# Kernel optimization log

Measured on AMD Instinct MI355X. Metric: run time of the kernel, lower is better.

The kernel has to match this reference:

```python
import jax, jax.numpy as jnp
import numpy as np

D = 256      # embedding_dim
K = 1024     # num_embeddings
B, S = 32, 2048

def setup_inputs() -> dict:
    key = jax.random.key(0)
    k1, k2 = jax.random.split(key)
    inp = jax.random.normal(k1, (B, S, D), dtype=jnp.float32)
    w = jax.random.normal(k2, (D, K), dtype=jnp.float32)  # codebook, [D, K]
    return {"input": inp, "w": w, "weights_loss": 0}


def reference(input, w, weights_loss):
    # flatten tokens: [N, D]
    flat = input.reshape(-1, D)
    N = flat.shape[0]
    # squared euclidean distances to each code: [N, K]
    distances = (jnp.sum(flat * flat, axis=1, keepdims=True)
                 - 2.0 * (flat @ w)
                 + jnp.sum(w * w, axis=0, keepdims=True))
    # nearest code per token (argmax of -dist == argmin of dist)
    flat_idx = jnp.argmax(-distances, axis=1)              # [N] int
    idx = flat_idx.reshape(input.shape[:-1])               # [B, S]
    # embedding gather: w.T is [K, D]
    quantize = jnp.take(w.T, idx, axis=0)                  # [B, S, D]
    # commitment loss: mse(stop_grad(quantize), flat_input)
    q_flat = quantize.reshape(-1, D)
    loss = jnp.mean((jax.lax.stop_gradient(q_flat) - flat) ** 2)
    # straight-through estimator
    quantize_st = input + jax.lax.stop_gradient(quantize - input)
    # one-hot statistics without materializing [N, K]
    dema_cluster_size = jax.ops.segment_sum(
        jnp.ones((N,), dtype=flat.dtype), flat_idx, num_segments=K)  # [K]
    dw = jax.ops.segment_sum(flat, flat_idx, num_segments=K).T       # [D, K]
    avg_probs = dema_cluster_size / N
    perplexity = jnp.exp(-jnp.sum(avg_probs * jnp.log(avg_probs + 1e-10)))
    return (loss,
            quantize_st,
            dema_cluster_size.reshape(1, K),
            dw.reshape(1, D, K),
            idx,
            perplexity)
```

## Files before the change

kernel.cpp:

```cpp
#include <hip/hip_runtime.h>


#define D 256
#define K 1024
#define NTOK 65536

#define OFF_Q   ((size_t)1)
#define OFF_CS  ((size_t)1 + (size_t)NTOK * D)
#define OFF_DW  (OFF_CS + K)
#define OFF_IDX (OFF_DW + (size_t)D * K)
#define OFF_P   (OFF_IDX + NTOK)

#define FLAG_TH  0.05f
#define FLAG_CAP 8192

typedef __attribute__((ext_vector_type(8))) short short8;
typedef __attribute__((ext_vector_type(16))) float f32x16;

__device__ __forceinline__ unsigned short f2bf(float f) {
  unsigned u = __float_as_uint(f);
  return (unsigned short)((u + 0x7FFFu + ((u >> 16) & 1u)) >> 16);
}
__device__ __forceinline__ float bf2f(unsigned short h) {
  return __uint_as_float(((unsigned)h) << 16);
}

__global__ __launch_bounds__(256) void prep_w(const float* __restrict__ w,
                                              float* __restrict__ wT,
                                              unsigned short* __restrict__ whG,
                                              unsigned short* __restrict__ wlG) {
  __shared__ float tile[32][33];
  const int k0 = blockIdx.x * 32, d0 = blockIdx.y * 32;
  const int tx = threadIdx.x, ty = threadIdx.y;
#pragma unroll
  for (int j = 0; j < 4; ++j) {
    const int r = ty + j * 8;
    tile[r][tx] = w[(size_t)(d0 + r) * K + k0 + tx];
  }
  __syncthreads();
#pragma unroll
  for (int j = 0; j < 4; ++j) {
    const int r = ty + j * 8;
    const int k = k0 + r, d = d0 + tx;
    const float v = tile[tx][r];
    wT[(size_t)k * D + d] = v;
    const unsigned short h = f2bf(v);
    const unsigned short l = f2bf(v - bf2f(h));
    const size_t idx = (size_t)(k >> 5) * 8192 +
                       (size_t)(((d >> 4) * 2 + ((d >> 3) & 1)) * 32 + (k & 31)) * 8 +
                       (d & 7);
    whG[idx] = h;
    wlG[idx] = l;
  }
}

__global__ __launch_bounds__(256) void wsq_kernel(const float* __restrict__ wT,
                                                  float* __restrict__ wsq) {
  const int wave = threadIdx.x >> 6, lane = threadIdx.x & 63;
  const int k = blockIdx.x * 4 + wave;
  const float4 v = *(const float4*)(wT + (size_t)k * D + lane * 4);
  float s = v.x * v.x + v.y * v.y + v.z * v.z + v.w * v.w;
#pragma unroll
  for (int m = 1; m < 64; m <<= 1) s += __shfl_xor(s, m);
  if (lane == 0) wsq[k] = s;
}

__global__ __launch_bounds__(256, 2) void vq_score(
    const float* __restrict__ x,
    const unsigned short* __restrict__ whG, const unsigned short* __restrict__ wlG,
    const float* __restrict__ wsq, float* __restrict__ out,
    int* __restrict__ idxInt, int* __restrict__ flagCnt, int* __restrict__ flagged) {
  __shared__ short whS[2][8192];
  __shared__ short wlS[2][8192];
  __shared__ float swsq[K];

  const int tid = threadIdx.x;
#pragma unroll
  for (int j = 0; j < 4; ++j) swsq[tid + j * 256] = wsq[tid + j * 256];

  const int wv = tid >> 6, lane = tid & 63;
  const int col = lane & 31, hi = lane >> 5;
  const int rowG = blockIdx.x * 128 + wv * 32 + col;

  short8 ah[16], al[16];
  {
    const float* xr = x + (size_t)rowG * D + hi * 8;
#pragma unroll
    for (int s = 0; s < 16; ++s) {
      const float4 f0 = *(const float4*)(xr + s * 16);
      const float4 f1 = *(const float4*)(xr + s * 16 + 4);
      const float fv[8] = {f0.x, f0.y, f0.z, f0.w, f1.x, f1.y, f1.z, f1.w};
      short8 a, b;
#pragma unroll
      for (int e = 0; e < 8; ++e) {
        const unsigned short h = f2bf(fv[e]);
        a[e] = (short)h;
        b[e] = (short)f2bf(fv[e] - bf2f(h));
      }
      ah[s] = a;
      al[s] = b;
    }
  }

  auto stage = [&](int chunk, int buf) {
    const short8* srcH = (const short8*)(whG + (size_t)chunk * 8192);
    const short8* srcL = (const short8*)(wlG + (size_t)chunk * 8192);
    short8* dstH = (short8*)whS[buf];
    short8* dstL = (short8*)wlS[buf];
#pragma unroll
    for (int j = 0; j < 4; ++j) {
      dstH[tid + j * 256] = srcH[tid + j * 256];
      dstL[tid + j * 256] = srcL[tid + j * 256];
    }
  };

  float s1[16], s2[16];
  int i1[16];
#pragma unroll
  for (int r = 0; r < 16; ++r) { s1[r] = -3.4e38f; s2[r] = -3.4e38f; i1[r] = 0; }

  stage(0, 0);
  __syncthreads();

  for (int chunk = 0; chunk < 32; ++chunk) {
    const int cur = chunk & 1;
    if (chunk + 1 < 32) stage(chunk + 1, cur ^ 1);

    const short* bhB = whS[cur];
    const short* blB = wlS[cur];
    f32x16 ahh, ahl, alh;
#pragma unroll
    for (int r = 0; r < 16; ++r) { ahh[r] = 0.f; ahl[r] = 0.f; alh[r] = 0.f; }
#pragma unroll
    for (int s = 0; s < 16; ++s) {
      const int off = ((s * 2 + hi) << 8) + (col << 3);
      const short8 bh = *(const short8*)(bhB + off);
      const short8 bl = *(const short8*)(blB + off);
      ahh = __builtin_amdgcn_mfma_f32_32x32x16_bf16(ah[s], bh, ahh, 0, 0, 0);
      ahl = __builtin_amdgcn_mfma_f32_32x32x16_bf16(ah[s], bl, ahl, 0, 0, 0);
      alh = __builtin_amdgcn_mfma_f32_32x32x16_bf16(al[s], bh, alh, 0, 0, 0);
    }

    const int cc = chunk * 32 + col;
    const float wq = swsq[cc];
#pragma unroll
    for (int r = 0; r < 16; ++r) {
      const float sc = fmaf(2.f, ahh[r] + ahl[r] + alh[r], -wq);
      const bool gt = sc > s1[r];
      s2[r] = fmaxf(s2[r], gt ? s1[r] : sc);
      if (gt) { s1[r] = sc; i1[r] = cc; }
    }
    __syncthreads();
  }

#pragma unroll
  for (int m = 1; m <= 16; m <<= 1) {
#pragma unroll
    for (int r = 0; r < 16; ++r) {
      const float os1 = __shfl_xor(s1[r], m);
      const int   oi1 = __shfl_xor(i1[r], m);
      const float os2 = __shfl_xor(s2[r], m);
      const bool take = (os1 > s1[r]) || (os1 == s1[r] && oi1 < i1[r]);
      const float loser = take ? s1[r] : os1;
      if (take) { s1[r] = os1; i1[r] = oi1; }
      s2[r] = fmaxf(fmaxf(s2[r], os2), loser);
    }
  }

  if (col == 0) {
    const size_t tb = (size_t)blockIdx.x * 128 + wv * 32;
#pragma unroll
    for (int r = 0; r < 16; ++r) {
      const int row = (r & 3) + 8 * (r >> 2) + 4 * hi;
      const size_t g = tb + row;
      idxInt[g] = i1[r];
      out[OFF_IDX + g] = (float)i1[r];
      if (s1[r] - s2[r] < FLAG_TH) {
        const int slot = atomicAdd(flagCnt, 1);
        if (slot < FLAG_CAP) flagged[slot] = (int)g;
      }
    }
  }
}

__global__ __launch_bounds__(256) void vq_fixup(
    const float* __restrict__ x, const float* __restrict__ wT,
    const float* __restrict__ wsq, const int* __restrict__ flagCnt,
    const int* __restrict__ flagged, unsigned long long* __restrict__ keyBuf) {
  __shared__ float ws32[32 * 264];
  __shared__ float xs[D];
  __shared__ unsigned long long wred[4];
  const int tid = threadIdx.x;
  const int cc = blockIdx.x & 31, j0 = blockIdx.x >> 5;
#pragma unroll
  for (int r = 0; r < 32; ++r)
    ws32[r * 264 + tid] = wT[(size_t)(cc * 32 + r) * D + tid];
  int F = *flagCnt;
  if (F > FLAG_CAP) F = FLAG_CAP;
  const int ci = tid >> 3, dg = tid & 7, c = cc * 32 + ci;
  const float wq = wsq[c];

  for (int slot = j0; slot < F; slot += 64) {
    const int t = flagged[slot];
    __syncthreads();
    xs[tid] = x[(size_t)t * D + tid];
    __syncthreads();
    float dot = 0.f;
#pragma unroll
    for (int i = 0; i < 32; ++i)
      dot = fmaf(xs[dg + 8 * i], ws32[ci * 264 + dg + 8 * i], dot);
    dot += __shfl_xor(dot, 1);
    dot += __shfl_xor(dot, 2);
    dot += __shfl_xor(dot, 4);
    unsigned long long key = 0ull;
    if (dg == 0) {
      const float sc = fmaf(2.f, dot, -wq);
      unsigned u = __float_as_uint(sc);
      u = (u & 0x80000000u) ? ~u : (u | 0x80000000u);
      key = ((unsigned long long)u << 32) | (unsigned)(1023 - c);
    }
#pragma unroll
    for (int m = 8; m <= 32; m <<= 1) {
      const unsigned long long o = __shfl_xor(key, m);
      if (o > key) key = o;
    }
    if ((tid & 63) == 0) wred[tid >> 6] = key;
    __syncthreads();
    if (tid == 0) {
      unsigned long long b = wred[0];
      if (wred[1] > b) b = wred[1];
      if (wred[2] > b) b = wred[2];
      if (wred[3] > b) b = wred[3];
      keyBuf[(size_t)slot * 32 + cc] = b;
    }
  }
}

__global__ __launch_bounds__(256) void vq_fixfin(
    const int* __restrict__ flagCnt, const int* __restrict__ flagged,
    const unsigned long long* __restrict__ keyBuf, int* __restrict__ idxInt,
    float* __restrict__ out) {
  int F = *flagCnt;
  if (F > FLAG_CAP) F = FLAG_CAP;
  for (int slot = blockIdx.x * 256 + threadIdx.x; slot < F; slot += 4096) {
    unsigned long long b = 0ull;
#pragma unroll
    for (int j = 0; j < 32; ++j) {
      const unsigned long long v = keyBuf[(size_t)slot * 32 + j];
      if (v > b) b = v;
    }
    const int c = 1023 - (int)(b & 0xFFFFFFFFull);
    const int t = flagged[slot];
    idxInt[t] = c;
    out[OFF_IDX + t] = (float)c;
  }
}

__global__ __launch_bounds__(256) void vq_count(const int* __restrict__ idxInt,
                                                int* __restrict__ countsInt) {
  const int t = blockIdx.x * 256 + threadIdx.x;
  atomicAdd(countsInt + idxInt[t], 1);
}

__global__ __launch_bounds__(1024) void vq_scan(const int* __restrict__ countsInt,
                                                int* __restrict__ bucketStart,
                                                int* __restrict__ cursorInt,
                                                float* __restrict__ out) {
  __shared__ int sc[1024];
  const int tid = threadIdx.x;
  const int c = countsInt[tid];
  out[OFF_CS + tid] = (float)c;
  sc[tid] = c;
  __syncthreads();
  for (int off = 1; off < 1024; off <<= 1) {
    int v = 0;
    if (tid >= off) v = sc[tid - off];
    __syncthreads();
    if (tid >= off) sc[tid] += v;
    __syncthreads();
  }
  bucketStart[tid] = sc[tid] - c;
  cursorInt[tid] = 0;
}

__global__ __launch_bounds__(256) void vq_scatter(const int* __restrict__ idxInt,
                                                  const int* __restrict__ bucketStart,
                                                  int* __restrict__ cursorInt,
                                                  int* __restrict__ sortedTok) {
  const int t = blockIdx.x * 256 + threadIdx.x;
  const int k = idxInt[t];
  const int pos = atomicAdd(cursorInt + k, 1);
  sortedTok[bucketStart[k] + pos] = t;
}

__global__ __launch_bounds__(256) void vq_process(
    const float* __restrict__ x, const float* __restrict__ wT,
    const int* __restrict__ countsInt, const int* __restrict__ bucketStart,
    const int* __restrict__ sortedTok, float* __restrict__ out,
    float* __restrict__ dwT, float* __restrict__ lossAcc) {
  __shared__ float sRed[4];
  const int tid = threadIdx.x;
  const int k = blockIdx.x >> 3, j = blockIdx.x & 7;
  const int cnt = countsInt[k], start = bucketStart[k];
  const int lo = start + ((cnt * j) >> 3);
  const int hiP = start + ((cnt * (j + 1)) >> 3);
  if (lo >= hiP) return;
  const float wv = wT[(size_t)k * D + tid];
  float acc = 0.f, lp = 0.f;
  int t = sortedTok[lo];
  for (int p = lo; p < hiP; ++p) {
    const int tn = (p + 1 < hiP) ? sortedTok[p + 1] : 0;
    const float xv = x[(size_t)t * D + tid];
    out[OFF_Q + (size_t)t * D + tid] = wv;
    acc += xv;
    const float dl = wv - xv;
    lp = fmaf(dl, dl, lp);
    t = tn;
  }
  atomicAdd(dwT + (size_t)k * D + tid, acc);
  const int wave = tid >> 6, lane = tid & 63;
#pragma unroll
  for (int m = 1; m < 64; m <<= 1) lp += __shfl_xor(lp, m);
  if (lane == 0) sRed[wave] = lp;
  __syncthreads();
  if (tid == 0) atomicAdd(lossAcc, sRed[0] + sRed[1] + sRed[2] + sRed[3]);
}

__global__ __launch_bounds__(256) void transpose_dw(const float* __restrict__ dwT,
                                                    float* __restrict__ out) {
  __shared__ float tile[32][33];
  const int d0 = blockIdx.x * 32, k0 = blockIdx.y * 32;
  const int tx = threadIdx.x, ty = threadIdx.y;
#pragma unroll
  for (int j = 0; j < 4; ++j) {
    const int r = ty + j * 8;
    tile[r][tx] = dwT[(size_t)(k0 + r) * D + d0 + tx];
  }
  __syncthreads();
#pragma unroll
  for (int j = 0; j < 4; ++j) {
    const int r = ty + j * 8;
    out[OFF_DW + (size_t)(d0 + r) * K + k0 + tx] = tile[tx][r];
  }
}

__global__ __launch_bounds__(1024) void finalize_kernel(const float* __restrict__ lossAcc,
                                                        float* __restrict__ out) {
  __shared__ float red[16];
  const int tid = threadIdx.x;
  const float c = out[OFF_CS + tid];
  const float avg = c * (1.0f / (float)NTOK);
  float term = avg * logf(avg + 1e-10f);
#pragma unroll
  for (int m = 1; m < 64; m <<= 1) term += __shfl_xor(term, m);
  const int wave = tid >> 6, lane = tid & 63;
  if (lane == 0) red[wave] = term;
  __syncthreads();
  if (tid == 0) {
    float s = 0.f;
#pragma unroll
    for (int i = 0; i < 16; ++i) s += red[i];
    out[OFF_P] = expf(-s);
    out[0] = lossAcc[0] * (1.0f / ((float)NTOK * (float)D));
  }
}

extern "C" void kernel_launch(void* const* d_in, const int* in_sizes, int n_in,
                              void* d_out, int out_size, void* d_ws, size_t ws_size,
                              hipStream_t stream) {
  const float* x = (const float*)d_in[0];
  const float* w = (const float*)d_in[1];
  float* out = (float*)d_out;
  char* wsb = (char*)d_ws;

  float* lossAcc   = (float*)(wsb + 0);
  int*   flagCnt   = (int*)(wsb + 4);
  float* wsq       = (float*)(wsb + 256);
  int*   countsInt = (int*)(wsb + 8192);
  int*   bucketStart = (int*)(wsb + 12288);
  int*   cursorInt = (int*)(wsb + 16384);
  int*   idxInt    = (int*)(wsb + 20480);
  int*   sortedTok = (int*)(wsb + 282624);
  int*   flagged   = (int*)(wsb + 544768);
  unsigned long long* keyBuf = (unsigned long long*)(wsb + 577536);
  float* wT        = (float*)(wsb + 2674688);
  unsigned short* whG = (unsigned short*)(wsb + 3723264);
  unsigned short* wlG = (unsigned short*)(wsb + 4247552);
  float* dwT       = (float*)(wsb + 4771840);

  hipMemsetAsync(wsb, 0, 16384, stream);
  hipMemsetAsync(dwT, 0, sizeof(float) * (size_t)K * D, stream);

  prep_w<<<dim3(K / 32, D / 32), dim3(32, 8), 0, stream>>>(w, wT, whG, wlG);
  wsq_kernel<<<dim3(K / 4), dim3(256), 0, stream>>>(wT, wsq);
  vq_score<<<dim3(NTOK / 128), dim3(256), 0, stream>>>(x, whG, wlG, wsq, out,
                                                       idxInt, flagCnt, flagged);
  vq_fixup<<<dim3(2048), dim3(256), 0, stream>>>(x, wT, wsq, flagCnt, flagged, keyBuf);
  vq_fixfin<<<dim3(16), dim3(256), 0, stream>>>(flagCnt, flagged, keyBuf, idxInt, out);
  vq_count<<<dim3(NTOK / 256), dim3(256), 0, stream>>>(idxInt, countsInt);
  vq_scan<<<dim3(1), dim3(1024), 0, stream>>>(countsInt, bucketStart, cursorInt, out);
  vq_scatter<<<dim3(NTOK / 256), dim3(256), 0, stream>>>(idxInt, bucketStart,
                                                         cursorInt, sortedTok);
  vq_process<<<dim3(K * 8), dim3(256), 0, stream>>>(x, wT, countsInt, bucketStart,
                                                    sortedTok, out, dwT, lossAcc);
  transpose_dw<<<dim3(D / 32, K / 32), dim3(32, 8), 0, stream>>>(dwT, out);
  finalize_kernel<<<dim3(1), dim3(1024), 0, stream>>>(lossAcc, out);
}
```

Measured before the change: 464.0 us.

## Fuse quantize write and counting into score kernel, async LDS staging, rework dw pass

The score kernel now stages codebook chunks with global_load_lds into one interleaved hi/lo buffer and issues the first stage before converting x. It also counts codes atomically and writes the quantized rows directly, so the separate count kernel goes away. The fixup finalizer now reduces keys per wave, corrects counts, and rewrites quantize rows only where the chosen index changed. The per-bucket process kernel becomes a dw/loss kernel over fixed 16-token groups of sorted tokens that flushes atomics whenever the code changes, and the fixup grid is resized. Together these are meant to cut launches and redundant memory traffic and to balance uneven buckets, at the cost of more atomics and a redundant quantize write for tokens later corrected.

```diff
diff --git a/kernel.cpp b/kernel.cpp
--- a/kernel.cpp
+++ b/kernel.cpp
@@ -25,10 +25,15 @@
   return __uint_as_float(((unsigned)h) << 16);
 }
 
+__device__ __forceinline__ void gload_lds16(void* g, void* l) {
+  __builtin_amdgcn_global_load_lds(
+      (__attribute__((address_space(1))) unsigned int*)g,
+      (__attribute__((address_space(3))) unsigned int*)l, 16, 0, 0);
+}
+
 __global__ __launch_bounds__(256) void prep_w(const float* __restrict__ w,
                                               float* __restrict__ wT,
-                                              unsigned short* __restrict__ whG,
-                                              unsigned short* __restrict__ wlG) {
+                                              unsigned short* __restrict__ wBG) {
   __shared__ float tile[32][33];
   const int k0 = blockIdx.x * 32, d0 = blockIdx.y * 32;
   const int tx = threadIdx.x, ty = threadIdx.y;
@@ -46,11 +51,11 @@
     wT[(size_t)k * D + d] = v;
     const unsigned short h = f2bf(v);
     const unsigned short l = f2bf(v - bf2f(h));
-    const size_t idx = (size_t)(k >> 5) * 8192 +
-                       (size_t)(((d >> 4) * 2 + ((d >> 3) & 1)) * 32 + (k & 31)) * 8 +
-                       (d & 7);
-    whG[idx] = h;
-    wlG[idx] = l;
+    const size_t frag = (size_t)(((d >> 4) * 2 + ((d >> 3) & 1)) * 32 + (k & 31)) * 8 +
+                        (d & 7);
+    const size_t base = (size_t)(k >> 5) * 16384;
+    wBG[base + frag] = h;
+    wBG[base + 8192 + frag] = l;
   }
 }
 
@@ -66,12 +71,11 @@
 }
 
 __global__ __launch_bounds__(256, 2) void vq_score(
-    const float* __restrict__ x,
-    const unsigned short* __restrict__ whG, const unsigned short* __restrict__ wlG,
-    const float* __restrict__ wsq, float* __restrict__ out,
-    int* __restrict__ idxInt, int* __restrict__ flagCnt, int* __restrict__ flagged) {
-  __shared__ short whS[2][8192];
-  __shared__ short wlS[2][8192];
+    const float* __restrict__ x, unsigned short* __restrict__ wBG,
+    const float* __restrict__ wsq, const float* __restrict__ wT,
+    float* __restrict__ out, int* __restrict__ idxInt, int* __restrict__ countsInt,
+    int* __restrict__ flagCnt, int* __restrict__ flagged) {
+  __shared__ short sB[2][16384];
   __shared__ float swsq[K];
 
   const int tid = threadIdx.x;
@@ -81,6 +85,16 @@
   const int wv = tid >> 6, lane = tid & 63;
   const int col = lane & 31, hi = lane >> 5;
   const int rowG = blockIdx.x * 128 + wv * 32 + col;
+
+  auto stage = [&](int chunk, int buf) {
+    unsigned short* src = wBG + (size_t)chunk * 16384 + wv * 4096 + lane * 8;
+    short* dst = &sB[buf][wv * 4096];
+#pragma unroll
+    for (int j = 0; j < 8; ++j)
+      gload_lds16(src + j * 512, dst + j * 512);
+  };
+
+  stage(0, 0);
 
   short8 ah[16], al[16];
   {
@@ -102,32 +116,19 @@
     }
   }
 
-  auto stage = [&](int chunk, int buf) {
-    const short8* srcH = (const short8*)(whG + (size_t)chunk * 8192);
-    const short8* srcL = (const short8*)(wlG + (size_t)chunk * 8192);
-    short8* dstH = (short8*)whS[buf];
-    short8* dstL = (short8*)wlS[buf];
-#pragma unroll
-    for (int j = 0; j < 4; ++j) {
-      dstH[tid + j * 256] = srcH[tid + j * 256];
-      dstL[tid + j * 256] = srcL[tid + j * 256];
-    }
-  };
-
   float s1[16], s2[16];
   int i1[16];
 #pragma unroll
   for (int r = 0; r < 16; ++r) { s1[r] = -3.4e38f; s2[r] = -3.4e38f; i1[r] = 0; }
 
-  stage(0, 0);
   __syncthreads();
 
   for (int chunk = 0; chunk < 32; ++chunk) {
     const int cur = chunk & 1;
     if (chunk + 1 < 32) stage(chunk + 1, cur ^ 1);
 
-    const short* bhB = whS[cur];
-    const short* blB = wlS[cur];
+    const short* bhB = sB[cur];
+    const short* blB = sB[cur] + 8192;
     f32x16 ahh, ahl, alh;
 #pragma unroll
     for (int r = 0; r < 16; ++r) { ahh[r] = 0.f; ahl[r] = 0.f; alh[r] = 0.f; }
@@ -167,19 +168,35 @@
     }
   }
 
+  const size_t tb = (size_t)blockIdx.x * 128 + wv * 32;
+
   if (col == 0) {
-    const size_t tb = (size_t)blockIdx.x * 128 + wv * 32;
 #pragma unroll
     for (int r = 0; r < 16; ++r) {
       const int row = (r & 3) + 8 * (r >> 2) + 4 * hi;
       const size_t g = tb + row;
       idxInt[g] = i1[r];
       out[OFF_IDX + g] = (float)i1[r];
+      atomicAdd(countsInt + i1[r], 1);
       if (s1[r] - s2[r] < FLAG_TH) {
         const int slot = atomicAdd(flagCnt, 1);
         if (slot < FLAG_CAP) flagged[slot] = (int)g;
       }
     }
+  }
+
+  const int l32 = lane & 31;
+#pragma unroll
+  for (int r = 0; r < 16; ++r) {
+    const int row = (r & 3) + 8 * (r >> 2) + 4 * hi;
+    const size_t t = tb + row;
+    const int k = i1[r];
+    const float* wrow = wT + (size_t)k * D + l32 * 8;
+    const float4 q0 = *(const float4*)(wrow);
+    const float4 q1 = *(const float4*)(wrow + 4);
+    float* od = out + OFF_Q + t * D + l32 * 8;
+    od[0] = q0.x; od[1] = q0.y; od[2] = q0.z; od[3] = q0.w;
+    od[4] = q1.x; od[5] = q1.y; od[6] = q1.z; od[7] = q1.w;
   }
 }
 
@@ -200,7 +217,7 @@
   const int ci = tid >> 3, dg = tid & 7, c = cc * 32 + ci;
   const float wq = wsq[c];
 
-  for (int slot = j0; slot < F; slot += 64) {
+  for (int slot = j0; slot < F; slot += 16) {
     const int t = flagged[slot];
     __syncthreads();
     xs[tid] = x[(size_t)t * D + tid];
@@ -239,27 +256,33 @@
 __global__ __launch_bounds__(256) void vq_fixfin(
     const int* __restrict__ flagCnt, const int* __restrict__ flagged,
     const unsigned long long* __restrict__ keyBuf, int* __restrict__ idxInt,
+    int* __restrict__ countsInt, const float* __restrict__ wT,
     float* __restrict__ out) {
   int F = *flagCnt;
   if (F > FLAG_CAP) F = FLAG_CAP;
-  for (int slot = blockIdx.x * 256 + threadIdx.x; slot < F; slot += 4096) {
-    unsigned long long b = 0ull;
-#pragma unroll
-    for (int j = 0; j < 32; ++j) {
-      const unsigned long long v = keyBuf[(size_t)slot * 32 + j];
-      if (v > b) b = v;
-    }
-    const int c = 1023 - (int)(b & 0xFFFFFFFFull);
+  const int wv = threadIdx.x >> 6, lane = threadIdx.x & 63;
+  for (int slot = blockIdx.x * 4 + wv; slot < F; slot += 64) {
     const int t = flagged[slot];
-    idxInt[t] = c;
-    out[OFF_IDX + t] = (float)c;
-  }
-}
-
-__global__ __launch_bounds__(256) void vq_count(const int* __restrict__ idxInt,
-                                                int* __restrict__ countsInt) {
-  const int t = blockIdx.x * 256 + threadIdx.x;
-  atomicAdd(countsInt + idxInt[t], 1);
+    unsigned long long key = (lane < 32) ? keyBuf[(size_t)slot * 32 + lane] : 0ull;
+#pragma unroll
+    for (int m = 1; m <= 32; m <<= 1) {
+      const unsigned long long o = __shfl_xor(key, m);
+      if (o > key) key = o;
+    }
+    const int c = 1023 - (int)(key & 0xFFFFFFFFull);
+    const int old = idxInt[t];
+    if (c != old) {
+      if (lane == 0) {
+        idxInt[t] = c;
+        out[OFF_IDX + t] = (float)c;
+        atomicAdd(countsInt + old, -1);
+        atomicAdd(countsInt + c, 1);
+      }
+      const float4 q = *(const float4*)(wT + (size_t)c * D + lane * 4);
+      float* od = out + OFF_Q + (size_t)t * D + lane * 4;
+      od[0] = q.x; od[1] = q.y; od[2] = q.z; od[3] = q.w;
+    }
+  }
 }
 
 __global__ __launch_bounds__(1024) void vq_scan(const int* __restrict__ countsInt,
@@ -293,35 +316,50 @@
   sortedTok[bucketStart[k] + pos] = t;
 }
 
-__global__ __launch_bounds__(256) void vq_process(
+__global__ __launch_bounds__(256) void vq_dwloss(
     const float* __restrict__ x, const float* __restrict__ wT,
-    const int* __restrict__ countsInt, const int* __restrict__ bucketStart,
-    const int* __restrict__ sortedTok, float* __restrict__ out,
+    const int* __restrict__ idxInt, const int* __restrict__ sortedTok,
     float* __restrict__ dwT, float* __restrict__ lossAcc) {
   __shared__ float sRed[4];
-  const int tid = threadIdx.x;
-  const int k = blockIdx.x >> 3, j = blockIdx.x & 7;
-  const int cnt = countsInt[k], start = bucketStart[k];
-  const int lo = start + ((cnt * j) >> 3);
-  const int hiP = start + ((cnt * (j + 1)) >> 3);
-  if (lo >= hiP) return;
-  const float wv = wT[(size_t)k * D + tid];
-  float acc = 0.f, lp = 0.f;
-  int t = sortedTok[lo];
-  for (int p = lo; p < hiP; ++p) {
-    const int tn = (p + 1 < hiP) ? sortedTok[p + 1] : 0;
-    const float xv = x[(size_t)t * D + tid];
-    out[OFF_Q + (size_t)t * D + tid] = wv;
-    acc += xv;
-    const float dl = wv - xv;
-    lp = fmaf(dl, dl, lp);
-    t = tn;
-  }
-  atomicAdd(dwT + (size_t)k * D + tid, acc);
-  const int wave = tid >> 6, lane = tid & 63;
+  const int tid = threadIdx.x, wv = tid >> 6, lane = tid & 63;
+  const int g = blockIdx.x * 4 + wv;
+  const int p0 = g * 16;
+  const int tk = sortedTok[p0 + (lane & 15)];
+  const int kk = idxInt[tk];
+
+  int kcur = -1;
+  float4 acc = {0.f, 0.f, 0.f, 0.f};
+  float4 wv4 = {0.f, 0.f, 0.f, 0.f};
+  float lp = 0.f;
+#pragma unroll
+  for (int i = 0; i < 16; ++i) {
+    const int t = __shfl(tk, i);
+    const int k = __shfl(kk, i);
+    if (k != kcur) {
+      if (kcur >= 0) {
+        float* dr = dwT + (size_t)kcur * D + lane * 4;
+        atomicAdd(dr + 0, acc.x); atomicAdd(dr + 1, acc.y);
+        atomicAdd(dr + 2, acc.z); atomicAdd(dr + 3, acc.w);
+      }
+      acc = {0.f, 0.f, 0.f, 0.f};
+      wv4 = *(const float4*)(wT + (size_t)k * D + lane * 4);
+      kcur = k;
+    }
+    const float4 xv = *(const float4*)(x + (size_t)t * D + lane * 4);
+    acc.x += xv.x; acc.y += xv.y; acc.z += xv.z; acc.w += xv.w;
+    const float dx = wv4.x - xv.x, dy = wv4.y - xv.y;
+    const float dz = wv4.z - xv.z, dw = wv4.w - xv.w;
+    lp = fmaf(dx, dx, lp); lp = fmaf(dy, dy, lp);
+    lp = fmaf(dz, dz, lp); lp = fmaf(dw, dw, lp);
+  }
+  {
+    float* dr = dwT + (size_t)kcur * D + lane * 4;
+    atomicAdd(dr + 0, acc.x); atomicAdd(dr + 1, acc.y);
+    atomicAdd(dr + 2, acc.z); atomicAdd(dr + 3, acc.w);
+  }
 #pragma unroll
   for (int m = 1; m < 64; m <<= 1) lp += __shfl_xor(lp, m);
-  if (lane == 0) sRed[wave] = lp;
+  if (lane == 0) sRed[wv] = lp;
   __syncthreads();
   if (tid == 0) atomicAdd(lossAcc, sRed[0] + sRed[1] + sRed[2] + sRed[3]);
 }
@@ -373,36 +411,35 @@
   float* out = (float*)d_out;
   char* wsb = (char*)d_ws;
 
-  float* lossAcc   = (float*)(wsb + 0);
-  int*   flagCnt   = (int*)(wsb + 4);
-  float* wsq       = (float*)(wsb + 256);
-  int*   countsInt = (int*)(wsb + 8192);
-  int*   bucketStart = (int*)(wsb + 12288);
-  int*   cursorInt = (int*)(wsb + 16384);
-  int*   idxInt    = (int*)(wsb + 20480);
-  int*   sortedTok = (int*)(wsb + 282624);
-  int*   flagged   = (int*)(wsb + 544768);
+  float* lossAcc     = (float*)(wsb + 0);
+  int*   flagCnt     = (int*)(wsb + 4);
+  int*   countsInt   = (int*)(wsb + 4096);
+  int*   bucketStart = (int*)(wsb + 8192);
+  int*   cursorInt   = (int*)(wsb + 12288);
+  float* wsq         = (float*)(wsb + 16384);
+  int*   idxInt      = (int*)(wsb + 20480);
+  int*   sortedTok   = (int*)(wsb + 282624);
+  int*   flagged     = (int*)(wsb + 544768);
   unsigned long long* keyBuf = (unsigned long long*)(wsb + 577536);
-  float* wT        = (float*)(wsb + 2674688);
-  unsigned short* whG = (unsigned short*)(wsb + 3723264);
-  unsigned short* wlG = (unsigned short*)(wsb + 4247552);
-  float* dwT       = (float*)(wsb + 4771840);
-
-  hipMemsetAsync(wsb, 0, 16384, stream);
+  float* wT          = (float*)(wsb + 2674688);
+  unsigned short* wBG = (unsigned short*)(wsb + 3723264);
+  float* dwT         = (float*)(wsb + 4771840);
+
+  hipMemsetAsync(wsb, 0, 20480, stream);
   hipMemsetAsync(dwT, 0, sizeof(float) * (size_t)K * D, stream);
 
-  prep_w<<<dim3(K / 32, D / 32), dim3(32, 8), 0, stream>>>(w, wT, whG, wlG);
+  prep_w<<<dim3(K / 32, D / 32), dim3(32, 8), 0, stream>>>(w, wT, wBG);
   wsq_kernel<<<dim3(K / 4), dim3(256), 0, stream>>>(wT, wsq);
-  vq_score<<<dim3(NTOK / 128), dim3(256), 0, stream>>>(x, whG, wlG, wsq, out,
-                                                       idxInt, flagCnt, flagged);
-  vq_fixup<<<dim3(2048), dim3(256), 0, stream>>>(x, wT, wsq, flagCnt, flagged, keyBuf);
-  vq_fixfin<<<dim3(16), dim3(256), 0, stream>>>(flagCnt, flagged, keyBuf, idxInt, out);
-  vq_count<<<dim3(NTOK / 256), dim3(256), 0, stream>>>(idxInt, countsInt);
+  vq_score<<<dim3(NTOK / 128), dim3(256), 0, stream>>>(
+      x, wBG, wsq, wT, out, idxInt, countsInt, flagCnt, flagged);
+  vq_fixup<<<dim3(512), dim3(256), 0, stream>>>(x, wT, wsq, flagCnt, flagged, keyBuf);
+  vq_fixfin<<<dim3(16), dim3(256), 0, stream>>>(flagCnt, flagged, keyBuf, idxInt,
+                                                countsInt, wT, out);
   vq_scan<<<dim3(1), dim3(1024), 0, stream>>>(countsInt, bucketStart, cursorInt, out);
   vq_scatter<<<dim3(NTOK / 256), dim3(256), 0, stream>>>(idxInt, bucketStart,
                                                          cursorInt, sortedTok);
-  vq_process<<<dim3(K * 8), dim3(256), 0, stream>>>(x, wT, countsInt, bucketStart,
-                                                    sortedTok, out, dwT, lossAcc);
+  vq_dwloss<<<dim3(1024), dim3(256), 0, stream>>>(x, wT, idxInt, sortedTok,
+                                                  dwT, lossAcc);
   transpose_dw<<<dim3(D / 32, K / 32), dim3(32, 8), 0, stream>>>(dwT, out);
   finalize_kernel<<<dim3(1), dim3(1024), 0, stream>>>(lossAcc, out);
 }
```

After: 387.2 us. -16.6%, faster.
